# Kernel tuning notes

Measured on AMD Instinct MI355X. Metric: run time of the kernel, lower is better.

The kernel has to match this reference:

```python
import jax, jax.numpy as jnp
import numpy as np

B, T, C = 4, 2048, 2048
H = 16
DH = C // H  # 128
ROPE_BASE = 10000.0


def _rms_norm(x):
    eps = jnp.finfo(x.dtype).eps
    return x * jax.lax.rsqrt(jnp.mean(x * x, axis=-1, keepdims=True) + eps)


def _rope_tables(seq_len, dim, dtype):
    inv_freq = 1.0 / (ROPE_BASE ** (jnp.arange(0, dim, 2, dtype=jnp.float32) / dim))
    t = jnp.arange(seq_len, dtype=jnp.float32)
    freqs = jnp.outer(t, inv_freq)  # [T, dim/2]
    return jnp.cos(freqs).astype(dtype), jnp.sin(freqs).astype(dtype)


def _apply_rotary(x, cos, sin):
    # x: [B, T, H, DH]; cos/sin: [T, DH/2] broadcast over batch and heads
    d = x.shape[-1] // 2
    x1, x2 = x[..., :d], x[..., d:]
    c = cos[None, :, None, :]
    s = sin[None, :, None, :]
    y1 = x1 * c + x2 * s
    y2 = -x1 * s + x2 * c
    return jnp.concatenate([y1, y2], axis=-1).astype(x.dtype)


def setup_inputs() -> dict:
    key = jax.random.key(0)
    k0, k1, k2, k3, k4 = jax.random.split(key, 5)
    scale = 1.0 / np.sqrt(C)
    return {
        "residual": jax.random.normal(k0, (B, T, C), dtype=jnp.float32),
        "wq": jax.random.normal(k1, (C, C), dtype=jnp.float32) * scale,
        "wk": jax.random.normal(k2, (C, C), dtype=jnp.float32) * scale,
        "wv": jax.random.normal(k3, (C, C), dtype=jnp.float32) * scale,
        "wproj": jax.random.normal(k4, (C, C), dtype=jnp.float32) * scale,
    }


def reference(residual, wq, wk, wv, wproj):
    x = _rms_norm(residual)  # [B, T, C]
    # torch Linear: y = x @ W.T, W is [out, in]
    q = jnp.einsum('btc,dc->btd', x, wq).reshape(B, T, H, DH)
    k = jnp.einsum('btc,dc->btd', x, wk).reshape(B, T, H, DH)
    v = jnp.einsum('btc,dc->btd', x, wv).reshape(B, T, H, DH)
    # per-head QK RMSNorm
    q = _rms_norm(q)
    k = _rms_norm(k)
    cos, sin = _rope_tables(T, DH, residual.dtype)
    q = _apply_rotary(q, cos, sin)
    k = _apply_rotary(k, cos, sin)
    # causal attention, scale 1/sqrt(head_dim)
    scores = jnp.einsum('bqhd,bkhd->bhqk', q, k) / jnp.sqrt(jnp.asarray(DH, q.dtype))
    causal = jnp.tril(jnp.ones((T, T), dtype=bool))
    scores = jnp.where(causal[None, None], scores, jnp.asarray(-jnp.inf, scores.dtype))
    attn = jax.nn.softmax(scores, axis=-1)
    y = jnp.einsum('bhqk,bkhd->bqhd', attn, v).reshape(B, T, C)
    y = jnp.einsum('btc,dc->btd', y, wproj)
    return residual + y
```

## Files before the change

kernel.cpp:

```cpp
#include <hip/hip_runtime.h>
#include <hip/hip_bf16.h>

#define B_  4
#define T_  2048
#define C_  2048
#define H_  16
#define DH_ 128
#define MROWS (B_ * T_)

typedef unsigned short bf16;
typedef __attribute__((ext_vector_type(8))) short bf16x8;
typedef __attribute__((ext_vector_type(4))) float f32x4;

__device__ __forceinline__ float bf2f(bf16 h) {
    return __uint_as_float(((unsigned int)h) << 16);
}
__device__ __forceinline__ bf16 f2bf(float f) {
    unsigned int u = __float_as_uint(f);
    u = (u + 0x7fffu + ((u >> 16) & 1u)) >> 16;
    return (bf16)u;
}

__device__ __forceinline__ int swz8(int row, int col) {
    return col ^ ((row & 7) << 3);
}

__device__ __forceinline__ void gld16(const bf16* g, bf16* l) {
    __builtin_amdgcn_global_load_lds(
        (const __attribute__((address_space(1))) unsigned int*)(const unsigned int*)g,
        (__attribute__((address_space(3))) unsigned int*)(unsigned int*)l,
        16, 0, 0);
}

__global__ __launch_bounds__(256) void w2bf(const float* __restrict__ w, bf16* __restrict__ o) {
    const size_t i = ((size_t)blockIdx.x * 256 + threadIdx.x) * 8;
    float4 a = *(const float4*)(w + i);
    float4 b = *(const float4*)(w + i + 4);
    union { uint4 u; bf16 h[8]; } p;
    p.h[0] = f2bf(a.x); p.h[1] = f2bf(a.y); p.h[2] = f2bf(a.z); p.h[3] = f2bf(a.w);
    p.h[4] = f2bf(b.x); p.h[5] = f2bf(b.y); p.h[6] = f2bf(b.z); p.h[7] = f2bf(b.w);
    *(uint4*)(o + i) = p.u;
}

__global__ __launch_bounds__(256) void rmsnorm_x(const float* __restrict__ in,
                                                 bf16* __restrict__ outx) {
    const int row = blockIdx.x, tid = threadIdx.x;
    const size_t base = (size_t)row * C_ + tid * 8;
    float4 a = *(const float4*)(in + base);
    float4 b = *(const float4*)(in + base + 4);
    float f[8] = {a.x, a.y, a.z, a.w, b.x, b.y, b.z, b.w};
    float ss = 0.f;
#pragma unroll
    for (int i = 0; i < 8; ++i) ss += f[i] * f[i];
#pragma unroll
    for (int m = 32; m; m >>= 1) ss += __shfl_xor(ss, m, 64);
    __shared__ float red[4];
    if ((tid & 63) == 0) red[tid >> 6] = ss;
    __syncthreads();
    float tot = red[0] + red[1] + red[2] + red[3];
    float sc = rsqrtf(tot * (1.0f / (float)C_) + 1.1920929e-07f);
    union { uint4 u; bf16 h[8]; } o;
#pragma unroll
    for (int i = 0; i < 8; ++i) o.h[i] = f2bf(f[i] * sc);
    *(uint4*)(outx + base) = o.u;
}

__global__ __launch_bounds__(256, 2)
void gemm_qkv(const bf16* __restrict__ A,
              const bf16* __restrict__ Wq, const bf16* __restrict__ Wk, const bf16* __restrict__ Wv,
              bf16* __restrict__ Dq, bf16* __restrict__ Dk, bf16* __restrict__ Dvt) {
    __shared__ __align__(16) bf16 sA[128 * 64];
    __shared__ __align__(16) bf16 sB[3][128 * 64];
    const int tid = threadIdx.x;
    const int w = tid >> 6, L = tid & 63;
    const int lane15 = L & 15, quad = L >> 4;
    const int m0 = blockIdx.x * 128, n0 = blockIdx.y * 128;
    const int wm = w >> 1, wn = w & 1;

    const bf16* aptr[4];
    const bf16* bptr[3][4];
#pragma unroll
    for (int it = 0; it < 4; ++it) {
        int slot = it * 256 + tid;
        int row = slot >> 3;
        int ch = slot & 7;
        aptr[it] = A + (size_t)(m0 + row) * C_ + ch * 8;
        bptr[0][it] = Wq + (size_t)(n0 + row) * C_ + ch * 8;
        bptr[1][it] = Wk + (size_t)(n0 + row) * C_ + ch * 8;
        bptr[2][it] = Wv + (size_t)(n0 + row) * C_ + ch * 8;
    }

    f32x4 accq[4][4] = {}, acck[4][4] = {}, accv[4][4] = {};
#pragma unroll 1
    for (int kt = 0; kt < C_ / 64; ++kt) {
        __syncthreads();
#pragma unroll
        for (int it = 0; it < 4; ++it) {
            gld16(aptr[it], sA + (size_t)(it * 256 + w * 64) * 8);
            aptr[it] += 64;
        }
#pragma unroll
        for (int m = 0; m < 3; ++m)
#pragma unroll
            for (int it = 0; it < 4; ++it) {
                gld16(bptr[m][it], sB[m] + (size_t)(it * 256 + w * 64) * 8);
                bptr[m][it] += 64;
            }
        __syncthreads();
#pragma unroll
        for (int ks = 0; ks < 2; ++ks) {
            bf16x8 af[4];
#pragma unroll
            for (int i = 0; i < 4; ++i) {
                int ar = wm * 64 + i * 16 + lane15;
                af[i] = *(const bf16x8*)(sA + ar * 64 + (ks * 4 + quad) * 8);
            }
            {
                bf16x8 bfr[4];
#pragma unroll
                for (int i = 0; i < 4; ++i) {
                    int br = wn * 64 + i * 16 + lane15;
                    bfr[i] = *(const bf16x8*)(sB[0] + br * 64 + (ks * 4 + quad) * 8);
                }
#pragma unroll
                for (int i = 0; i < 4; ++i)
#pragma unroll
                    for (int j = 0; j < 4; ++j)
                        accq[i][j] = __builtin_amdgcn_mfma_f32_16x16x32_bf16(af[i], bfr[j], accq[i][j], 0, 0, 0);
            }
            {
                bf16x8 bfr[4];
#pragma unroll
                for (int i = 0; i < 4; ++i) {
                    int br = wn * 64 + i * 16 + lane15;
                    bfr[i] = *(const bf16x8*)(sB[1] + br * 64 + (ks * 4 + quad) * 8);
                }
#pragma unroll
                for (int i = 0; i < 4; ++i)
#pragma unroll
                    for (int j = 0; j < 4; ++j)
                        acck[i][j] = __builtin_amdgcn_mfma_f32_16x16x32_bf16(af[i], bfr[j], acck[i][j], 0, 0, 0);
            }
            {
                bf16x8 bfr[4];
#pragma unroll
                for (int i = 0; i < 4; ++i) {
                    int br = wn * 64 + i * 16 + lane15;
                    bfr[i] = *(const bf16x8*)(sB[2] + br * 64 + (ks * 4 + quad) * 8);
                }
#pragma unroll
                for (int i = 0; i < 4; ++i)
#pragma unroll
                    for (int j = 0; j < 4; ++j)
                        accv[i][j] = __builtin_amdgcn_mfma_f32_16x16x32_bf16(af[i], bfr[j], accv[i][j], 0, 0, 0);
            }
        }
    }

#pragma unroll
    for (int i = 0; i < 4; ++i)
#pragma unroll
        for (int j = 0; j < 4; ++j)
#pragma unroll
            for (int r = 0; r < 4; ++r) {
                int row = m0 + wm * 64 + i * 16 + quad * 4 + r;
                int col = n0 + wn * 64 + j * 16 + lane15;
                Dq[(size_t)row * C_ + col] = f2bf(accq[i][j][r]);
                Dk[(size_t)row * C_ + col] = f2bf(acck[i][j][r]);
            }
#pragma unroll
    for (int i = 0; i < 4; ++i) {
        int t0 = m0 + wm * 64 + i * 16 + quad * 4;
        int bidx = t0 >> 11, tin = t0 & (T_ - 1);
#pragma unroll
        for (int j = 0; j < 4; ++j) {
            int col = n0 + wn * 64 + j * 16 + lane15;
            int hh = col >> 7, dh = col & (DH_ - 1);
            unsigned int lo = (unsigned int)f2bf(accv[i][j][0]) | ((unsigned int)f2bf(accv[i][j][1]) << 16);
            unsigned int hi = (unsigned int)f2bf(accv[i][j][2]) | ((unsigned int)f2bf(accv[i][j][3]) << 16);
            uint2 val; val.x = lo; val.y = hi;
            *(uint2*)(Dvt + ((size_t)((bidx * H_ + hh) * DH_ + dh)) * T_ + tin) = val;
        }
    }
}

__global__ __launch_bounds__(256, 2)
void gemm_proj(const bf16* __restrict__ A, const bf16* __restrict__ W,
               float* __restrict__ D, const float* __restrict__ Add) {
    __shared__ __align__(16) bf16 sA[128 * 64];
    __shared__ __align__(16) bf16 sB[128 * 64];
    const int tid = threadIdx.x;
    const int w = tid >> 6, L = tid & 63;
    const int lane15 = L & 15, quad = L >> 4;
    const int m0 = blockIdx.x * 128, n0 = blockIdx.y * 128;
    const int wm = w >> 1, wn = w & 1;

    const bf16* aptr[4];
    const bf16* bptr[4];
#pragma unroll
    for (int it = 0; it < 4; ++it) {
        int slot = it * 256 + tid;
        int row = slot >> 3;
        int ch = slot & 7;
        aptr[it] = A + (size_t)(m0 + row) * C_ + ch * 8;
        bptr[it] = W + (size_t)(n0 + row) * C_ + ch * 8;
    }

    f32x4 acc[4][4] = {};
#pragma unroll 1
    for (int kt = 0; kt < C_ / 64; ++kt) {
        __syncthreads();
#pragma unroll
        for (int it = 0; it < 4; ++it) {
            gld16(aptr[it], sA + (size_t)(it * 256 + w * 64) * 8);
            aptr[it] += 64;
        }
#pragma unroll
        for (int it = 0; it < 4; ++it) {
            gld16(bptr[it], sB + (size_t)(it * 256 + w * 64) * 8);
            bptr[it] += 64;
        }
        __syncthreads();
#pragma unroll
        for (int ks = 0; ks < 2; ++ks) {
            bf16x8 af[4], bfr[4];
#pragma unroll
            for (int i = 0; i < 4; ++i) {
                int ar = wm * 64 + i * 16 + lane15;
                af[i]  = *(const bf16x8*)(sA + ar * 64 + (ks * 4 + quad) * 8);
                int br = wn * 64 + i * 16 + lane15;
                bfr[i] = *(const bf16x8*)(sB + br * 64 + (ks * 4 + quad) * 8);
            }
#pragma unroll
            for (int i = 0; i < 4; ++i)
#pragma unroll
                for (int j = 0; j < 4; ++j)
                    acc[i][j] = __builtin_amdgcn_mfma_f32_16x16x32_bf16(af[i], bfr[j], acc[i][j], 0, 0, 0);
        }
    }

#pragma unroll
    for (int i = 0; i < 4; ++i)
#pragma unroll
        for (int j = 0; j < 4; ++j)
#pragma unroll
            for (int r = 0; r < 4; ++r) {
                int row = m0 + wm * 64 + i * 16 + quad * 4 + r;
                int col = n0 + wn * 64 + j * 16 + lane15;
                D[(size_t)row * C_ + col] = acc[i][j][r] + Add[(size_t)row * C_ + col];
            }
}

__global__ __launch_bounds__(256) void qknorm_rope(bf16* __restrict__ q, bf16* __restrict__ k) {
    const int bt = blockIdx.x;
    bf16* buf = blockIdx.y ? k : q;
    const int w = threadIdx.x >> 6, L = threadIdx.x & 63;
    const int t = bt & (T_ - 1);
    float inv = (float)exp2(-(double)L * 0.20762050593046006);
    float ang = (float)t * inv;
    float s, c;
    sincosf(ang, &s, &c);
#pragma unroll
    for (int hh = 0; hh < 4; ++hh) {
        int h = w * 4 + hh;
        bf16* p = buf + (size_t)bt * C_ + h * DH_;
        float x1 = bf2f(p[L]), x2 = bf2f(p[L + 64]);
        float ss = x1 * x1 + x2 * x2;
#pragma unroll
        for (int m = 32; m; m >>= 1) ss += __shfl_xor(ss, m, 64);
        float sc = rsqrtf(ss * (1.0f / (float)DH_) + 1.1920929e-07f);
        float y1 = (x1 * c + x2 * s) * sc;
        float y2 = (x2 * c - x1 * s) * sc;
        p[L]      = f2bf(y1);
        p[L + 64] = f2bf(y2);
    }
}

__global__ __launch_bounds__(256, 2)
void attn_fwd(const bf16* __restrict__ q, const bf16* __restrict__ k,
              const bf16* __restrict__ vt, bf16* __restrict__ y) {
    __shared__ __align__(16) bf16 sKP[128 * 128];
    __shared__ __align__(16) bf16 sV[128 * 128];
    const int qt = blockIdx.x, bh = blockIdx.y;
    const int b = bh >> 4, h = bh & 15;
    const int tid = threadIdx.x;
    const int w = tid >> 6, L = tid & 63;
    const int lane15 = L & 15, quad = L >> 4;
    const float SCALE = 0.08838834764831845f;

    bf16x8 qf[2][4];
#pragma unroll
    for (int nt = 0; nt < 2; ++nt)
#pragma unroll
        for (int ks = 0; ks < 4; ++ks) {
            int qrow = qt * 128 + w * 32 + nt * 16 + lane15;
            qf[nt][ks] = *(const bf16x8*)(q + ((size_t)(b * T_ + qrow)) * C_ + h * DH_ + ks * 32 + quad * 8);
        }

    f32x4 o[2][8] = {};
    float m_i[2] = {-__builtin_inff(), -__builtin_inff()};
    float l_i[2] = {0.f, 0.f};

    for (int j = 0; j <= qt; ++j) {
        __syncthreads();
        {
            const bf16* kb = k  + ((size_t)(b * T_ + j * 128)) * C_ + h * DH_;
            const bf16* vb = vt + ((size_t)bh * DH_) * T_ + j * 128;
#pragma unroll
            for (int it = 0; it < 8; ++it) {
                int slot = it * 256 + tid;
                int row = slot >> 4;
                int ch = slot & 15;
                bf16x8 kv = *(const bf16x8*)(kb + (size_t)row * C_ + ch * 8);
                bf16x8 vv = *(const bf16x8*)(vb + (size_t)row * T_ + ch * 8);
                *(bf16x8*)(sKP + row * 128 + swz8(row, ch * 8)) = kv;
                *(bf16x8*)(sV  + row * 128 + swz8(row, ch * 8)) = vv;
            }
        }
        __syncthreads();

        f32x4 sc[8][2] = {};
#pragma unroll
        for (int ks = 0; ks < 4; ++ks)
#pragma unroll
            for (int mt = 0; mt < 8; ++mt) {
                int ar = mt * 16 + lane15;
                bf16x8 a = *(const bf16x8*)(sKP + ar * 128 + swz8(ar, (ks * 4 + quad) * 8));
                sc[mt][0] = __builtin_amdgcn_mfma_f32_16x16x32_bf16(a, qf[0][ks], sc[mt][0], 0, 0, 0);
                sc[mt][1] = __builtin_amdgcn_mfma_f32_16x16x32_bf16(a, qf[1][ks], sc[mt][1], 0, 0, 0);
            }

        float alpha[2];
#pragma unroll
        for (int nt = 0; nt < 2; ++nt) {
            const int qr = qt * 128 + w * 32 + nt * 16 + lane15;
            float mx = -__builtin_inff();
#pragma unroll
            for (int mt = 0; mt < 8; ++mt)
#pragma unroll
                for (int r = 0; r < 4; ++r) {
                    float v = sc[mt][nt][r] * SCALE;
                    if (j == qt) {
                        int kr = j * 128 + mt * 16 + quad * 4 + r;
                        if (kr > qr) v = -__builtin_inff();
                    }
                    sc[mt][nt][r] = v;
                    mx = fmaxf(mx, v);
                }
            mx = fmaxf(mx, __shfl_xor(mx, 16));
            mx = fmaxf(mx, __shfl_xor(mx, 32));
            float mn = fmaxf(m_i[nt], mx);
            alpha[nt] = __expf(m_i[nt] - mn);
            float sum = 0.f;
#pragma unroll
            for (int mt = 0; mt < 8; ++mt)
#pragma unroll
                for (int r = 0; r < 4; ++r) {
                    float p = __expf(sc[mt][nt][r] - mn);
                    sc[mt][nt][r] = p;
                    sum += p;
                }
            sum += __shfl_xor(sum, 16);
            sum += __shfl_xor(sum, 32);
            l_i[nt] = l_i[nt] * alpha[nt] + sum;
            m_i[nt] = mn;
        }

        __syncthreads();

#pragma unroll
        for (int mt = 0; mt < 8; ++mt)
#pragma unroll
            for (int nt = 0; nt < 2; ++nt) {
                int prow = w * 32 + nt * 16 + lane15;
                int kr0 = mt * 16 + quad * 4;
                int off = prow * 128 + swz8(prow, kr0);
                unsigned int lo = (unsigned int)f2bf(sc[mt][nt][0]) | ((unsigned int)f2bf(sc[mt][nt][1]) << 16);
                unsigned int hi = (unsigned int)f2bf(sc[mt][nt][2]) | ((unsigned int)f2bf(sc[mt][nt][3]) << 16);
                uint2 val; val.x = lo; val.y = hi;
                *(uint2*)(sKP + off) = val;
            }

#pragma unroll
        for (int mt = 0; mt < 2; ++mt)
#pragma unroll
            for (int r = 0; r < 4; ++r) {
                float av = __shfl(alpha[mt], quad * 4 + r, 64);
#pragma unroll
                for (int d = 0; d < 8; ++d) o[mt][d][r] *= av;
            }

        __syncthreads();

#pragma unroll
        for (int ks = 0; ks < 4; ++ks) {
            bf16x8 ap[2];
#pragma unroll
            for (int mt = 0; mt < 2; ++mt) {
                int pr = w * 32 + mt * 16 + lane15;
                ap[mt] = *(const bf16x8*)(sKP + pr * 128 + swz8(pr, (ks * 4 + quad) * 8));
            }
#pragma unroll
            for (int d = 0; d < 8; ++d) {
                int vr = d * 16 + lane15;
                bf16x8 bv = *(const bf16x8*)(sV + vr * 128 + swz8(vr, (ks * 4 + quad) * 8));
                o[0][d] = __builtin_amdgcn_mfma_f32_16x16x32_bf16(ap[0], bv, o[0][d], 0, 0, 0);
                o[1][d] = __builtin_amdgcn_mfma_f32_16x16x32_bf16(ap[1], bv, o[1][d], 0, 0, 0);
            }
        }
    }

    float rl[2] = {1.f / l_i[0], 1.f / l_i[1]};
#pragma unroll
    for (int mt = 0; mt < 2; ++mt)
#pragma unroll
        for (int r = 0; r < 4; ++r) {
            float linv = __shfl(rl[mt], quad * 4 + r, 64);
            int t = qt * 128 + w * 32 + mt * 16 + quad * 4 + r;
#pragma unroll
            for (int d = 0; d < 8; ++d)
                y[((size_t)(b * T_ + t)) * C_ + h * DH_ + d * 16 + lane15] = f2bf(o[mt][d][r] * linv);
        }
}

extern "C" void kernel_launch(void* const* d_in, const int* in_sizes, int n_in,
                              void* d_out, int out_size, void* d_ws, size_t ws_size,
                              hipStream_t stream) {
    const float* residual = (const float*)d_in[0];
    const float* wq    = (const float*)d_in[1];
    const float* wk    = (const float*)d_in[2];
    const float* wv    = (const float*)d_in[3];
    const float* wproj = (const float*)d_in[4];

    const size_t NE = (size_t)B_ * T_ * C_;
    const size_t WE = (size_t)C_ * C_;
    bf16* x  = (bf16*)d_ws;
    bf16* q  = x + NE;
    bf16* vt = q + NE;
    bf16* kk = (bf16*)d_out;
    bf16* wqb = kk + NE;
    bf16* wkb = wqb + WE;
    bf16* wvb = wkb + WE;
    bf16* y  = x;
    bf16* wpb = q;

    const dim3 gemm_grid(MROWS / 128, C_ / 128);
    const int wgrid = (int)(WE / (256 * 8));

    w2bf<<<wgrid, 256, 0, stream>>>(wq, wqb);
    w2bf<<<wgrid, 256, 0, stream>>>(wk, wkb);
    w2bf<<<wgrid, 256, 0, stream>>>(wv, wvb);
    rmsnorm_x<<<MROWS, 256, 0, stream>>>(residual, x);
    gemm_qkv<<<gemm_grid, 256, 0, stream>>>(x, wqb, wkb, wvb, q, kk, vt);
    qknorm_rope<<<dim3(MROWS, 2), 256, 0, stream>>>(q, kk);
    attn_fwd<<<dim3(T_ / 128, B_ * H_), 256, 0, stream>>>(q, kk, vt, y);
    w2bf<<<wgrid, 256, 0, stream>>>(wproj, wpb);
    gemm_proj<<<gemm_grid, 256, 0, stream>>>(y, wpb, (float*)d_out, residual);
}
```

Measured before the change: 682.8 us.

## Use exp2 softmax with lazy rescaling, drop a barrier, fuse weight casts

The attention softmax now folds log2(e) into the score scale and calls the hardware exp2 directly. It also skips rescaling the running max and output accumulator unless some lane's new max exceeds the old one by more than a threshold. The barrier between writing P to shared memory and the PV product is removed, which relies on each wave reading back only the rows it wrote. The three separate weight-to-bf16 conversion launches are merged into one kernel with a 3-row grid. Lazy rescaling lets unnormalized probabilities grow up to about 2^11.5, which stays within fp32 and bf16 range but slightly changes rounding.

Result: slower. 777.1 us (+13.8%).

```diff
diff --git a/kernel.cpp b/kernel.cpp
--- a/kernel.cpp
+++ b/kernel.cpp
@@ -30,6 +30,20 @@
         (const __attribute__((address_space(1))) unsigned int*)(const unsigned int*)g,
         (__attribute__((address_space(3))) unsigned int*)(unsigned int*)l,
         16, 0, 0);
+}
+
+__global__ __launch_bounds__(256) void w2bf3(const float* __restrict__ w0, const float* __restrict__ w1,
+                                             const float* __restrict__ w2, bf16* __restrict__ o0,
+                                             bf16* __restrict__ o1, bf16* __restrict__ o2) {
+    const float* w = blockIdx.y == 0 ? w0 : (blockIdx.y == 1 ? w1 : w2);
+    bf16* o = blockIdx.y == 0 ? o0 : (blockIdx.y == 1 ? o1 : o2);
+    const size_t i = ((size_t)blockIdx.x * 256 + threadIdx.x) * 8;
+    float4 a = *(const float4*)(w + i);
+    float4 b = *(const float4*)(w + i + 4);
+    union { uint4 u; bf16 h[8]; } p;
+    p.h[0] = f2bf(a.x); p.h[1] = f2bf(a.y); p.h[2] = f2bf(a.z); p.h[3] = f2bf(a.w);
+    p.h[4] = f2bf(b.x); p.h[5] = f2bf(b.y); p.h[6] = f2bf(b.z); p.h[7] = f2bf(b.w);
+    *(uint4*)(o + i) = p.u;
 }
 
 __global__ __launch_bounds__(256) void w2bf(const float* __restrict__ w, bf16* __restrict__ o) {
@@ -286,7 +300,7 @@
     const int tid = threadIdx.x;
     const int w = tid >> 6, L = tid & 63;
     const int lane15 = L & 15, quad = L >> 4;
-    const float SCALE = 0.08838834764831845f;
+    const float SCL2E = 0.08838834764831845f * 1.4426950408889634f;
 
     bf16x8 qf[2][4];
 #pragma unroll
@@ -331,6 +345,7 @@
             }
 
         float alpha[2];
+        bool needv[2];
 #pragma unroll
         for (int nt = 0; nt < 2; ++nt) {
             const int qr = qt * 128 + w * 32 + nt * 16 + lane15;
@@ -339,7 +354,7 @@
             for (int mt = 0; mt < 8; ++mt)
 #pragma unroll
                 for (int r = 0; r < 4; ++r) {
-                    float v = sc[mt][nt][r] * SCALE;
+                    float v = sc[mt][nt][r] * SCL2E;
                     if (j == qt) {
                         int kr = j * 128 + mt * 16 + quad * 4 + r;
                         if (kr > qr) v = -__builtin_inff();
@@ -349,14 +364,16 @@
                 }
             mx = fmaxf(mx, __shfl_xor(mx, 16));
             mx = fmaxf(mx, __shfl_xor(mx, 32));
-            float mn = fmaxf(m_i[nt], mx);
-            alpha[nt] = __expf(m_i[nt] - mn);
+            bool nd = __any(mx > m_i[nt] + 11.5f) != 0;
+            float mn = nd ? fmaxf(m_i[nt], mx) : m_i[nt];
+            alpha[nt] = nd ? __builtin_amdgcn_exp2f(m_i[nt] - mn) : 1.0f;
+            needv[nt] = nd;
             float sum = 0.f;
 #pragma unroll
             for (int mt = 0; mt < 8; ++mt)
 #pragma unroll
                 for (int r = 0; r < 4; ++r) {
-                    float p = __expf(sc[mt][nt][r] - mn);
+                    float p = __builtin_amdgcn_exp2f(sc[mt][nt][r] - mn);
                     sc[mt][nt][r] = p;
                     sum += p;
                 }
@@ -382,15 +399,15 @@
             }
 
 #pragma unroll
-        for (int mt = 0; mt < 2; ++mt)
-#pragma unroll
-            for (int r = 0; r < 4; ++r) {
-                float av = __shfl(alpha[mt], quad * 4 + r, 64);
-#pragma unroll
-                for (int d = 0; d < 8; ++d) o[mt][d][r] *= av;
-            }
-
-        __syncthreads();
+        for (int g = 0; g < 2; ++g)
+            if (needv[g]) {
+#pragma unroll
+                for (int r = 0; r < 4; ++r) {
+                    float av = __shfl(alpha[g], quad * 4 + r, 64);
+#pragma unroll
+                    for (int d = 0; d < 8; ++d) o[g][d][r] *= av;
+                }
+            }
 
 #pragma unroll
         for (int ks = 0; ks < 4; ++ks) {
@@ -447,9 +464,7 @@
     const dim3 gemm_grid(MROWS / 128, C_ / 128);
     const int wgrid = (int)(WE / (256 * 8));
 
-    w2bf<<<wgrid, 256, 0, stream>>>(wq, wqb);
-    w2bf<<<wgrid, 256, 0, stream>>>(wk, wkb);
-    w2bf<<<wgrid, 256, 0, stream>>>(wv, wvb);
+    w2bf3<<<dim3(wgrid, 3), 256, 0, stream>>>(wq, wk, wv, wqb, wkb, wvb);
     rmsnorm_x<<<MROWS, 256, 0, stream>>>(residual, x);
     gemm_qkv<<<gemm_grid, 256, 0, stream>>>(x, wqb, wkb, wvb, q, kk, vt);
     qknorm_rope<<<dim3(MROWS, 2), 256, 0, stream>>>(q, kk);
```
